# Kernel tuning notes

Measured on AMD Instinct MI355X. Metric: run time of the kernel, lower is better.

The kernel has to match this reference:

```python
import jax, jax.numpy as jnp
import numpy as np

WINDOW_SIZE = 2
SOFTMAX_TEMP = 0.01
CART_RESOLUTION = 0.25
RANGE_KEEP = 3.0
EPS = 1e-12


def get_indices(batch_size, window_size):
    kp, dense = [], []
    for i in range(batch_size):
        for j in range(window_size - 1):
            kp.append(i * window_size + j)
            dense.append(i * window_size + j + 1)
    return np.asarray(kp), np.asarray(dense)


def normalize_coords(coords, height, width):
    # coords [B,N,2] pixel (u,v) -> [-1,1] (align_corners=True convention, as in the repo)
    u = 2.0 * coords[..., 0] / (width - 1) - 1.0
    v = 2.0 * coords[..., 1] / (height - 1) - 1.0
    return jnp.stack([u, v], axis=-1)


def grid_sample_bilinear(img, grid):
    # Matches torch F.grid_sample(mode='bilinear', padding_mode='zeros', align_corners=False)
    # img [B,C,H,W], grid [B,Hg,Wg,2] with (x,y) in [-1,1]
    B, C, H, W = img.shape
    x = ((grid[..., 0] + 1.0) * W - 1.0) * 0.5
    y = ((grid[..., 1] + 1.0) * H - 1.0) * 0.5
    x0 = jnp.floor(x); y0 = jnp.floor(y)
    wx1 = x - x0; wy1 = y - y0

    def gather(xi, yi):
        valid = (xi >= 0) & (xi <= W - 1) & (yi >= 0) & (yi <= H - 1)
        xc = jnp.clip(xi, 0, W - 1).astype(jnp.int32)
        yc = jnp.clip(yi, 0, H - 1).astype(jnp.int32)
        v = jax.vmap(lambda im, yy, xx: im[:, yy, xx])(img, yc, xc)  # [B,C,Hg,Wg]
        return v * valid[:, None].astype(img.dtype)

    x1 = x0 + 1.0; y1 = y0 + 1.0
    out = (gather(x0, y0) * ((1.0 - wx1) * (1.0 - wy1))[:, None]
           + gather(x1, y0) * (wx1 * (1.0 - wy1))[:, None]
           + gather(x0, y1) * ((1.0 - wx1) * wy1)[:, None]
           + gather(x1, y1) * (wx1 * wy1)[:, None])
    return out


def setup_inputs() -> dict:
    key = jax.random.key(0)
    k1, k2, k3, k4, k5 = jax.random.split(key, 5)
    BW, C, N, H, W = 4, 256, 1024, 256, 256
    return {
        "keypoint_scores": jax.random.uniform(k1, (BW, 1, N), jnp.float32),
        "keypoint_desc": jax.random.normal(k2, (BW, C, N), jnp.float32),
        "scores_dense": jax.random.uniform(k3, (BW, 1, H, W), jnp.float32),
        "desc_dense": jax.random.normal(k4, (BW, C, H, W), jnp.float32),
        "keypoint_coords": jax.random.uniform(k5, (BW, N, 2), jnp.float32) * (W - 1),
    }


def reference(keypoint_scores, keypoint_desc, scores_dense, desc_dense, keypoint_coords):
    BW, encoder_dim, n_points = keypoint_desc.shape
    batch_size = BW // WINDOW_SIZE
    _, _, height, width = desc_dense.shape
    kp_inds, dense_inds = get_indices(batch_size, WINDOW_SIZE)

    src_coords = keypoint_coords[kp_inds]                      # [B,N,2]
    src_desc = keypoint_desc[kp_inds]                          # [B,C,N]
    src_desc = src_desc / jnp.maximum(jnp.linalg.norm(src_desc, axis=1, keepdims=True), EPS)
    B = src_desc.shape[0]

    tgt_desc_dense = desc_dense[dense_inds]                    # [B,C,H,W]
    tgt = tgt_desc_dense.reshape(B, encoder_dim, height * width)
    tgt = tgt / jnp.maximum(jnp.linalg.norm(tgt, axis=1, keepdims=True), EPS)

    # dense correlation [B, n_points, H*W]
    match_vals = jnp.einsum('bcn,bcm->bnm', src_desc, tgt)

    # local window mask (vectorized equivalent of the B x n_points python loop)
    keep_range = int(RANGE_KEEP // CART_RESOLUTION + 1)
    uv = jax.lax.stop_gradient(jnp.trunc(src_coords)).astype(jnp.int32)  # [B,N,2]
    u = uv[..., 0][..., None]   # [B,N,1]
    v = uv[..., 1][..., None]
    vg = jnp.arange(height)[None, None, :]
    ug = jnp.arange(width)[None, None, :]
    vmask = (vg >= v - keep_range) & (vg <= v + keep_range)    # [B,N,H]
    umask = (ug >= u - keep_range) & (ug <= u + keep_range)    # [B,N,W]
    mask = (vmask[..., :, None] & umask[..., None, :]).reshape(B, n_points, height * width)
    match_vals = match_vals * mask.astype(match_vals.dtype)

    soft = jax.nn.softmax(match_vals / SOFTMAX_TEMP, axis=2)   # [B,N,HW]

    # soft-argmax over the dense grid (meshgrid 'ij': v over rows, u over cols)
    ucoord = jnp.tile(jnp.arange(width, dtype=jnp.float32), height)
    vcoord = jnp.repeat(jnp.arange(height, dtype=jnp.float32), width)
    coords = jnp.stack([ucoord, vcoord], axis=1)               # [HW,2]
    pseudo_coords = jnp.einsum('bnm,mc->bnc', soft, coords)    # [B,N,2]

    pseudo_norm = normalize_coords(pseudo_coords, height, width)[:, None]  # [B,1,N,2]

    tgt_scores_dense = scores_dense[dense_inds]                # [B,1,H,W]
    pseudo_scores = grid_sample_bilinear(tgt_scores_dense, pseudo_norm).reshape(B, 1, n_points)
    pseudo_desc = grid_sample_bilinear(tgt_desc_dense, pseudo_norm).reshape(B, encoder_dim, n_points)

    desc_match_score = jnp.sum(src_desc * pseudo_desc, axis=1, keepdims=True) / float(encoder_dim)
    src_scores = keypoint_scores[kp_inds]
    match_weights = 0.5 * (desc_match_score + 1.0) * src_scores * pseudo_scores  # score_comp=True

    return pseudo_coords, match_weights, jnp.asarray(kp_inds)
```

## Files before the change

### kernel.cpp

```cpp
#include <hip/hip_runtime.h>
#include <math.h>

#define HH 256
#define WW 256
#define CC 256
#define HW 65536
#define NPTS 1024
#define BB 2
#define KEEP 13
#define KEEPM 14
#define TINV 100.0f
#define EPSN 1e-12f
#define S_ALL 8355840.0f

#define TW 32
#define TH 4
#define TUN 8
#define TPB 512
#define NT  (BB * TPB)
#define CAPT 192
#define VSTRIDE 864

__global__ __launch_bounds__(256) void prep_src(const float* __restrict__ kdesc,
                                                const float* __restrict__ kcoords,
                                                float* __restrict__ srcn,
                                                unsigned int* __restrict__ kparams) {
    int wid = threadIdx.x >> 6, lane = threadIdx.x & 63;
    int kpt = blockIdx.x * 4 + wid;
    int b = kpt >> 10, n = kpt & 1023;
    const float* src = kdesc + (size_t)(2 * b) * CC * NPTS + n;
    float vals[4];
    float ss = 0.f;
#pragma unroll
    for (int k = 0; k < 4; k++) {
        float x = src[(size_t)(lane + 64 * k) * NPTS];
        vals[k] = x;
        ss += x * x;
    }
    for (int o = 32; o > 0; o >>= 1) ss += __shfl_down(ss, o, 64);
    ss = __shfl(ss, 0, 64);
    float inv = 1.0f / fmaxf(sqrtf(ss), EPSN);
    float* dst = srcn + (size_t)kpt * CC;
#pragma unroll
    for (int k = 0; k < 4; k++) dst[lane + 64 * k] = vals[k] * inv;

    if (lane == 0) {
        float cu = kcoords[((size_t)(2 * b) * NPTS + n) * 2 + 0];
        float cv = kcoords[((size_t)(2 * b) * NPTS + n) * 2 + 1];
        int u = (int)truncf(cu), v = (int)truncf(cv);
        int u0m = max(0, u - KEEPM), u1m = min(WW - 1, u + KEEPM);
        int v0m = max(0, v - KEEPM), v1m = min(HH - 1, v + KEEPM);
        int nWm = u1m - u0m + 1, nHm = v1m - v0m + 1;
        kparams[kpt] = (unsigned)u0m | ((unsigned)v0m << 8) |
                       ((unsigned)nWm << 16) | ((unsigned)nHm << 24);
    }
}

__global__ __launch_bounds__(256) void corr_tiles(const float* __restrict__ ddense,
                                                  const float* __restrict__ srcn,
                                                  const unsigned int* __restrict__ kparams,
                                                  float* __restrict__ vals,
                                                  float* __restrict__ invn) {
    __shared__ float B_lds[CC][33];
    __shared__ int s_kid[CAPT];
    __shared__ unsigned int s_kp[CAPT];
    __shared__ int s_cnt;

    int tileg = blockIdx.x;
    int b = tileg >> 9, tl = tileg & 511;
    int tv = tl >> 3, tu = tl & 7;
    int vb = tv * TH, ub = tu * TW;
    int t = threadIdx.x;
    if (t == 0) s_cnt = 0;
    __syncthreads();

    for (int i = t; i < NPTS; i += 256) {
        unsigned int kp = kparams[b * NPTS + i];
        int u0m = kp & 255, v0m = (kp >> 8) & 255;
        int nWm = (kp >> 16) & 255, nHm = (int)(kp >> 24);
        if (u0m <= ub + TW - 1 && u0m + nWm - 1 >= ub &&
            v0m <= vb + TH - 1 && v0m + nHm - 1 >= vb) {
            int slot = atomicAdd(&s_cnt, 1);
            if (slot < CAPT) {
                s_kid[slot] = b * NPTS + i;
                s_kp[slot] = kp;
            }
        }
    }
    __syncthreads();
    int nk = min(s_cnt, CAPT);
    if (nk == 0) return;

    int pxg = t & 31, kg = t >> 5;
    int px4 = pxg * 4, k4 = kg * 4;
    const float* abase = ddense + (size_t)(2 * b + 1) * CC * HW +
                         (size_t)(vb + (px4 >> 5)) * WW + (ub + (px4 & 31));

    for (int kc = 0; kc < nk; kc += 32) {
        int nkk = min(32, nk - kc);
#pragma unroll 4
        for (int i = 0; i < nkk; i++)
            B_lds[t][i] = srcn[(size_t)s_kid[kc + i] * CC + t];
        __syncthreads();

        float acc[4][4];
#pragma unroll
        for (int i = 0; i < 4; i++)
#pragma unroll
            for (int j = 0; j < 4; j++) acc[i][j] = 0.f;

        int kgn = (nkk + 3) >> 2;
        if (kg < kgn) {
            float ss0 = 0.f, ss1 = 0.f, ss2 = 0.f, ss3 = 0.f;
#pragma unroll 4
            for (int c = 0; c < CC; c++) {
                float4 av = *(const float4*)(abase + (size_t)c * HW);
                const float* brow = &B_lds[c][k4];
                float b0 = brow[0], b1 = brow[1], b2 = brow[2], b3 = brow[3];
                acc[0][0] = fmaf(av.x, b0, acc[0][0]);
                acc[0][1] = fmaf(av.x, b1, acc[0][1]);
                acc[0][2] = fmaf(av.x, b2, acc[0][2]);
                acc[0][3] = fmaf(av.x, b3, acc[0][3]);
                acc[1][0] = fmaf(av.y, b0, acc[1][0]);
                acc[1][1] = fmaf(av.y, b1, acc[1][1]);
                acc[1][2] = fmaf(av.y, b2, acc[1][2]);
                acc[1][3] = fmaf(av.y, b3, acc[1][3]);
                acc[2][0] = fmaf(av.z, b0, acc[2][0]);
                acc[2][1] = fmaf(av.z, b1, acc[2][1]);
                acc[2][2] = fmaf(av.z, b2, acc[2][2]);
                acc[2][3] = fmaf(av.z, b3, acc[2][3]);
                acc[3][0] = fmaf(av.w, b0, acc[3][0]);
                acc[3][1] = fmaf(av.w, b1, acc[3][1]);
                acc[3][2] = fmaf(av.w, b2, acc[3][2]);
                acc[3][3] = fmaf(av.w, b3, acc[3][3]);
                ss0 = fmaf(av.x, av.x, ss0);
                ss1 = fmaf(av.y, av.y, ss1);
                ss2 = fmaf(av.z, av.z, ss2);
                ss3 = fmaf(av.w, av.w, ss3);
            }
            if (kc == 0 && kg == 0) {
                float i0 = 1.0f / fmaxf(sqrtf(ss0), EPSN);
                float i1 = 1.0f / fmaxf(sqrtf(ss1), EPSN);
                float i2 = 1.0f / fmaxf(sqrtf(ss2), EPSN);
                float i3 = 1.0f / fmaxf(sqrtf(ss3), EPSN);
                int wv = vb + (px4 >> 5), wu = ub + (px4 & 31);
                float* ip = invn + (size_t)b * HW + wv * WW + wu;
                ip[0] = i0; ip[1] = i1; ip[2] = i2; ip[3] = i3;
            }
        }

#pragma unroll
        for (int i = 0; i < 4; i++) {
            int px = px4 + i;
            int wv = vb + (px >> 5), wu = ub + (px & 31);
#pragma unroll
            for (int j = 0; j < 4; j++) {
                int s = k4 + j;
                if (s < nkk) {
                    unsigned int kp = s_kp[kc + s];
                    int u0m = kp & 255, v0m = (kp >> 8) & 255;
                    int nWm = (kp >> 16) & 255, nHm = (int)(kp >> 24);
                    int du = wu - u0m, dv = wv - v0m;
                    if ((unsigned)du < (unsigned)nWm && (unsigned)dv < (unsigned)nHm)
                        vals[(size_t)s_kid[kc + s] * VSTRIDE + dv * nWm + du] =
                            acc[i][j];
                }
            }
        }
        __syncthreads();
    }
}

__device__ inline float blockSum(float v, float* sred, int t) {
    for (int o = 32; o > 0; o >>= 1) v += __shfl_down(v, o, 64);
    __syncthreads();
    if ((t & 63) == 0) sred[t >> 6] = v;
    __syncthreads();
    return sred[0] + sred[1] + sred[2] + sred[3];
}

__global__ __launch_bounds__(256) void finish(const float* __restrict__ kscores,
                                              const float* __restrict__ sdense,
                                              const float* __restrict__ ddense,
                                              const float* __restrict__ kcoords,
                                              const float* __restrict__ srcn,
                                              const float* __restrict__ vals,
                                              const float* __restrict__ invn,
                                              float* __restrict__ out) {
    __shared__ float s_src[CC];
    __shared__ float s_red[4];
    int t = threadIdx.x;
    int kpt = blockIdx.x;
    int b = kpt >> 10, n = kpt & 1023;

    s_src[t] = srcn[(size_t)kpt * CC + t];

    float cu = kcoords[((size_t)(2 * b) * NPTS + n) * 2 + 0];
    float cv = kcoords[((size_t)(2 * b) * NPTS + n) * 2 + 1];
    int u = (int)truncf(cu), v = (int)truncf(cv);
    int u0 = max(0, u - KEEP), u1 = min(WW - 1, u + KEEP);
    int v0 = max(0, v - KEEP), v1 = min(HH - 1, v + KEEP);
    int nW = u1 - u0 + 1, nH = v1 - v0 + 1;
    int cnt = nW * nH;
    int u0m = max(0, u - KEEPM), u1m = min(WW - 1, u + KEEPM);
    int v0m = max(0, v - KEEPM), v1m = min(HH - 1, v + KEEPM);
    int nWm = u1m - u0m + 1, nHm = v1m - v0m + 1;
    int cntm = nWm * nHm;

    const float* vrow = vals + (size_t)kpt * VSTRIDE;
    const float* inb = invn + (size_t)b * HW;
    __syncthreads();

    float valk[4];
    int puk[4], pvk[4];
    bool gk[4];
    float lm = -INFINITY;
#pragma unroll
    for (int k = 0; k < 4; k++) {
        int p = t + k * 256;
        bool gm = p < cntm;
        int pp = gm ? p : 0;
        int dvm = pp / nWm, dum = pp - dvm * nWm;
        int pu = u0m + dum, pv = v0m + dvm;
        bool inw = gm && pu >= u0 && pu <= u1 && pv >= v0 && pv <= v1;
        float raw = gm ? vrow[pp] : 0.f;
        float val = inw ? raw * inb[pv * WW + pu] : 0.f;
        valk[k] = val;
        puk[k] = pu;
        pvk[k] = pv;
        gk[k] = inw;
        if (inw) lm = fmaxf(lm, val);
    }

    for (int o = 32; o > 0; o >>= 1) lm = fmaxf(lm, __shfl_down(lm, o, 64));
    if ((t & 63) == 0) s_red[t >> 6] = lm;
    __syncthreads();
    float m = fmaxf(fmaxf(s_red[0], s_red[1]), fmaxf(s_red[2], s_red[3]));
    m = fmaxf(m, 0.0f);

    float pse = 0.f, psu = 0.f, psv = 0.f;
#pragma unroll
    for (int k = 0; k < 4; k++) {
        float e = gk[k] ? expf(TINV * (valk[k] - m)) : 0.f;
        pse += e;
        psu = fmaf(e, (float)puk[k], psu);
        psv = fmaf(e, (float)pvk[k], psv);
    }
    float se = blockSum(pse, s_red, t);
    float su = blockSum(psu, s_red, t);
    float sv = blockSum(psv, s_red, t);

    float em = expf(-TINV * m);
    float sumWinU = 0.5f * (float)(u0 + u1) * (float)nW * (float)nH;
    float sumWinV = 0.5f * (float)(v0 + v1) * (float)nH * (float)nW;
    float denom = se + (65536.0f - (float)cnt) * em;
    float pcu = (su + em * (S_ALL - sumWinU)) / denom;
    float pcv = (sv + em * (S_ALL - sumWinV)) / denom;

    if (t == 0) {
        out[((size_t)b * NPTS + n) * 2 + 0] = pcu;
        out[((size_t)b * NPTS + n) * 2 + 1] = pcv;
    }

    float x = pcu * (256.0f / 255.0f) - 0.5f;
    float y = pcv * (256.0f / 255.0f) - 0.5f;
    float x0f = floorf(x), y0f = floorf(y);
    float wx = x - x0f, wy = y - y0f;
    int xi0 = (int)x0f, yi0 = (int)y0f, xi1 = xi0 + 1, yi1 = yi0 + 1;
    float w00 = (1.f - wx) * (1.f - wy), w10 = wx * (1.f - wy);
    float w01 = (1.f - wx) * wy, w11 = wx * wy;
    bool vx0 = (xi0 >= 0) & (xi0 < WW), vx1 = (xi1 >= 0) & (xi1 < WW);
    bool vy0 = (yi0 >= 0) & (yi0 < HH), vy1 = (yi1 >= 0) & (yi1 < HH);
    int cx0 = min(max(xi0, 0), WW - 1), cx1 = min(max(xi1, 0), WW - 1);
    int cy0 = min(max(yi0, 0), HH - 1), cy1 = min(max(yi1, 0), HH - 1);

    int cxs[4] = {cx0, cx1, cx0, cx1};
    int cys[4] = {cy0, cy0, cy1, cy1};
    bool cvalid[4] = {vx0 && vy0, vx1 && vy0, vx0 && vy1, vx1 && vy1};
    float wts[4] = {w00, w10, w01, w11};

    bool need = false;
    float dacc = 0.f;
#pragma unroll
    for (int c4 = 0; c4 < 4; c4++) {
        if (cvalid[c4]) {
            int du = cxs[c4] - u0m, dv = cys[c4] - v0m;
            if ((unsigned)du < (unsigned)nWm && (unsigned)dv < (unsigned)nHm)
                dacc = fmaf(wts[c4], vrow[dv * nWm + du], dacc);
            else
                need = true;
        }
    }

    float dms;
    if (need) {
        const float* tgt = ddense + (size_t)(2 * b + 1) * CC * HW;
        int c = t;
        const float* ch = tgt + ((size_t)c << 16);
        float d00 = cvalid[0] ? ch[cys[0] * WW + cxs[0]] : 0.f;
        float d10 = cvalid[1] ? ch[cys[1] * WW + cxs[1]] : 0.f;
        float d01 = cvalid[2] ? ch[cys[2] * WW + cxs[2]] : 0.f;
        float d11 = cvalid[3] ? ch[cys[3] * WW + cxs[3]] : 0.f;
        float pd = d00 * wts[0] + d10 * wts[1] + d01 * wts[2] + d11 * wts[3];
        float dsum = blockSum(pd * s_src[c], s_red, t);
        dms = dsum / (float)CC;
    } else {
        dms = dacc / (float)CC;
    }

    if (t == 0) {
        const float* sch = sdense + (size_t)(2 * b + 1) * HW;
        float s00 = cvalid[0] ? sch[cys[0] * WW + cxs[0]] : 0.f;
        float s10 = cvalid[1] ? sch[cys[1] * WW + cxs[1]] : 0.f;
        float s01 = cvalid[2] ? sch[cys[2] * WW + cxs[2]] : 0.f;
        float s11 = cvalid[3] ? sch[cys[3] * WW + cxs[3]] : 0.f;
        float psc = s00 * wts[0] + s10 * wts[1] + s01 * wts[2] + s11 * wts[3];
        float sscore = kscores[(size_t)(2 * b) * NPTS + n];
        float wgt = 0.5f * (dms + 1.0f) * sscore * psc;
        out[2 * NPTS * BB + (size_t)b * NPTS + n] = wgt;
    }

    if (kpt == 0 && t < 2) out[3 * NPTS * BB + t] = 2.0f * (float)t;
}

__global__ __launch_bounds__(256) void prep_tgt(const float* __restrict__ dd,
                                                float* __restrict__ invn) {
    int idx = blockIdx.x * 256 + threadIdx.x;
    int b = idx >> 16, m = idx & 65535;
    const float* p = dd + (size_t)(2 * b + 1) * CC * HW + m;
    float ss = 0.f;
#pragma unroll 4
    for (int c = 0; c < CC; c++) {
        float x = p[(size_t)c << 16];
        ss += x * x;
    }
    invn[idx] = 1.0f / fmaxf(sqrtf(ss), EPSN);
}

__global__ __launch_bounds__(256) void matcher(const float* __restrict__ kscores,
                                               const float* __restrict__ sdense,
                                               const float* __restrict__ ddense,
                                               const float* __restrict__ kcoords,
                                               const float* __restrict__ srcn,
                                               const float* __restrict__ invn,
                                               float* __restrict__ out) {
    __shared__ float s_src[CC];
    __shared__ float s_red[4];
    int t = threadIdx.x;
    int kpt = blockIdx.x;
    int b = kpt >> 10, n = kpt & 1023;

    s_src[t] = srcn[(size_t)kpt * CC + t];

    float cu = kcoords[((size_t)(2 * b) * NPTS + n) * 2 + 0];
    float cv = kcoords[((size_t)(2 * b) * NPTS + n) * 2 + 1];
    int u = (int)truncf(cu), v = (int)truncf(cv);
    int u0 = max(0, u - KEEP), u1 = min(WW - 1, u + KEEP);
    int v0 = max(0, v - KEEP), v1 = min(HH - 1, v + KEEP);
    int nW = u1 - u0 + 1, nH = v1 - v0 + 1;
    int cnt = nW * nH;

    const float* tgt = ddense + (size_t)(2 * b + 1) * CC * HW;
    const float* inb = invn + (size_t)b * HW;
    __syncthreads();

    int p0 = t, p1 = t + 256, p2 = t + 512;
    bool g0 = p0 < cnt, g1 = p1 < cnt, g2 = p2 < cnt;
    int dv0 = p0 / nW, dv1 = p1 / nW, dv2 = p2 / nW;
    int uu0 = u0 + (p0 - dv0 * nW), uu1 = u0 + (p1 - dv1 * nW), uu2 = u0 + (p2 - dv2 * nW);
    int vv0 = v0 + dv0, vv1 = v0 + dv1, vv2 = v0 + dv2;
    int mi0 = g0 ? (vv0 * WW + uu0) : 0;
    int mi1 = g1 ? (vv1 * WW + uu1) : 0;
    int mi2 = g2 ? (vv2 * WW + uu2) : 0;

    const float* q0 = tgt + mi0;
    const float* q1 = tgt + mi1;
    const float* q2 = tgt + mi2;
    float a0 = 0.f, a1 = 0.f, a2 = 0.f;
#pragma unroll 4
    for (int c = 0; c < CC; c++) {
        float s = s_src[c];
        size_t off = (size_t)c << 16;
        a0 = fmaf(s, q0[off], a0);
        a1 = fmaf(s, q1[off], a1);
        a2 = fmaf(s, q2[off], a2);
    }
    float val0 = a0 * inb[mi0];
    float val1 = a1 * inb[mi1];
    float val2 = a2 * inb[mi2];

    float lm = fmaxf(fmaxf(g0 ? val0 : -INFINITY, g1 ? val1 : -INFINITY),
                     g2 ? val2 : -INFINITY);
    for (int o = 32; o > 0; o >>= 1) lm = fmaxf(lm, __shfl_down(lm, o, 64));
    if ((t & 63) == 0) s_red[t >> 6] = lm;
    __syncthreads();
    float m = fmaxf(fmaxf(s_red[0], s_red[1]), fmaxf(s_red[2], s_red[3]));
    m = fmaxf(m, 0.0f);

    float e0 = g0 ? expf(TINV * (val0 - m)) : 0.f;
    float e1 = g1 ? expf(TINV * (val1 - m)) : 0.f;
    float e2 = g2 ? expf(TINV * (val2 - m)) : 0.f;

    float se = blockSum(e0 + e1 + e2, s_red, t);
    float su = blockSum(e0 * uu0 + e1 * uu1 + e2 * uu2, s_red, t);
    float sv = blockSum(e0 * vv0 + e1 * vv1 + e2 * vv2, s_red, t);

    float em = expf(-TINV * m);
    float sumWinU = 0.5f * (float)(u0 + u1) * (float)nW * (float)nH;
    float sumWinV = 0.5f * (float)(v0 + v1) * (float)nH * (float)nW;
    float denom = se + (65536.0f - (float)cnt) * em;
    float pcu = (su + em * (S_ALL - sumWinU)) / denom;
    float pcv = (sv + em * (S_ALL - sumWinV)) / denom;

    if (t == 0) {
        out[((size_t)b * NPTS + n) * 2 + 0] = pcu;
        out[((size_t)b * NPTS + n) * 2 + 1] = pcv;
    }

    float x = pcu * (256.0f / 255.0f) - 0.5f;
    float y = pcv * (256.0f / 255.0f) - 0.5f;
    float x0f = floorf(x), y0f = floorf(y);
    float wx = x - x0f, wy = y - y0f;
    int xi0 = (int)x0f, yi0 = (int)y0f, xi1 = xi0 + 1, yi1 = yi0 + 1;
    float w00 = (1.f - wx) * (1.f - wy), w10 = wx * (1.f - wy);
    float w01 = (1.f - wx) * wy, w11 = wx * wy;
    bool vx0 = (xi0 >= 0) & (xi0 < WW), vx1 = (xi1 >= 0) & (xi1 < WW);
    bool vy0 = (yi0 >= 0) & (yi0 < HH), vy1 = (yi1 >= 0) & (yi1 < HH);
    int cx0 = min(max(xi0, 0), WW - 1), cx1 = min(max(xi1, 0), WW - 1);
    int cy0 = min(max(yi0, 0), HH - 1), cy1 = min(max(yi1, 0), HH - 1);

    {
        int c = t;
        const float* ch = tgt + ((size_t)c << 16);
        float d00 = (vx0 && vy0) ? ch[cy0 * WW + cx0] : 0.f;
        float d10 = (vx1 && vy0) ? ch[cy0 * WW + cx1] : 0.f;
        float d01 = (vx0 && vy1) ? ch[cy1 * WW + cx0] : 0.f;
        float d11 = (vx1 && vy1) ? ch[cy1 * WW + cx1] : 0.f;
        float pd = d00 * w00 + d10 * w10 + d01 * w01 + d11 * w11;
        float contrib = pd * s_src[c];
        float dsum = blockSum(contrib, s_red, t);
        if (t == 0) {
            float dms = dsum / (float)CC;
            const float* sch = sdense + (size_t)(2 * b + 1) * HW;
            float s00 = (vx0 && vy0) ? sch[cy0 * WW + cx0] : 0.f;
            float s10 = (vx1 && vy0) ? sch[cy0 * WW + cx1] : 0.f;
            float s01 = (vx0 && vy1) ? sch[cy1 * WW + cx0] : 0.f;
            float s11 = (vx1 && vy1) ? sch[cy1 * WW + cx1] : 0.f;
            float psc = s00 * w00 + s10 * w10 + s01 * w01 + s11 * w11;
            float sscore = kscores[(size_t)(2 * b) * NPTS + n];
            float wgt = 0.5f * (dms + 1.0f) * sscore * psc;
            out[2 * NPTS * BB + (size_t)b * NPTS + n] = wgt;
        }
    }

    if (kpt == 0 && t < 2) out[3 * NPTS * BB + t] = 2.0f * (float)t;
}

extern "C" void kernel_launch(void* const* d_in, const int* in_sizes, int n_in,
                              void* d_out, int out_size, void* d_ws, size_t ws_size,
                              hipStream_t stream) {
    const float* kscores = (const float*)d_in[0];
    const float* kdesc   = (const float*)d_in[1];
    const float* sdense  = (const float*)d_in[2];
    const float* ddense  = (const float*)d_in[3];
    const float* kcoords = (const float*)d_in[4];
    float* out = (float*)d_out;

    float* srcn = (float*)d_ws;
    float* vals = srcn + (size_t)BB * NPTS * CC;
    float* invn = vals + (size_t)BB * NPTS * VSTRIDE;
    unsigned int* kparams = (unsigned int*)(invn + (size_t)BB * HW);
    size_t need = ((size_t)BB * NPTS * CC + (size_t)BB * NPTS * VSTRIDE +
                   (size_t)BB * HW + BB * NPTS) * 4;

    if (ws_size >= need) {
        hipLaunchKernelGGL(prep_src, dim3(512), dim3(256), 0, stream,
                           kdesc, kcoords, srcn, kparams);
        hipLaunchKernelGGL(corr_tiles, dim3(NT), dim3(256), 0, stream,
                           ddense, srcn, kparams, vals, invn);
        hipLaunchKernelGGL(finish, dim3(BB * NPTS), dim3(256), 0, stream,
                           kscores, sdense, ddense, kcoords, srcn, vals, invn, out);
    } else {
        float* invn2 = srcn + (size_t)BB * NPTS * CC;
        hipLaunchKernelGGL(prep_src, dim3(512), dim3(256), 0, stream,
                           kdesc, kcoords, srcn, kparams);
        hipLaunchKernelGGL(prep_tgt, dim3(512), dim3(256), 0, stream, ddense, invn2);
        hipLaunchKernelGGL(matcher, dim3(BB * NPTS), dim3(256), 0, stream,
                           kscores, sdense, ddense, kcoords, srcn, invn2, out);
    }
}
```

Baseline: 92.05 us.

## Bin keypoints to tiles globally and split correlation tiles into chunk blocks

Adds a bin_kpts kernel that uses global atomics to build a per-tile keypoint list once, replacing the per-block scan of all 1024 keypoints in corr_tiles. corr_tiles now launches one block per (tile, 32-keypoint chunk), so the serial chunk loop inside a block becomes parallel work. prep_src is rewritten to transpose 64 keypoints through LDS for coalesced loads and stores. The per-tile capacity drops from 192 to 96 keypoints, and the change adds a memset plus an extra kernel launch.

```diff
diff --git a/kernel.cpp b/kernel.cpp
--- a/kernel.cpp
+++ b/kernel.cpp
@@ -17,34 +17,47 @@
 #define TH 4
 #define TUN 8
 #define TPB 512
-#define NT  (BB * TPB)
-#define CAPT 192
+#define NTILE (BB * TPB)
+#define CAPL 96
+#define NCHUNK 3
 #define VSTRIDE 864
+#define BPAD 36
+#define KPB 64
 
 __global__ __launch_bounds__(256) void prep_src(const float* __restrict__ kdesc,
                                                 const float* __restrict__ kcoords,
                                                 float* __restrict__ srcn,
                                                 unsigned int* __restrict__ kparams) {
-    int wid = threadIdx.x >> 6, lane = threadIdx.x & 63;
-    int kpt = blockIdx.x * 4 + wid;
-    int b = kpt >> 10, n = kpt & 1023;
-    const float* src = kdesc + (size_t)(2 * b) * CC * NPTS + n;
-    float vals[4];
-    float ss = 0.f;
-#pragma unroll
-    for (int k = 0; k < 4; k++) {
-        float x = src[(size_t)(lane + 64 * k) * NPTS];
-        vals[k] = x;
-        ss += x * x;
-    }
-    for (int o = 32; o > 0; o >>= 1) ss += __shfl_down(ss, o, 64);
-    ss = __shfl(ss, 0, 64);
-    float inv = 1.0f / fmaxf(sqrtf(ss), EPSN);
-    float* dst = srcn + (size_t)kpt * CC;
-#pragma unroll
-    for (int k = 0; k < 4; k++) dst[lane + 64 * k] = vals[k] * inv;
-
-    if (lane == 0) {
+    __shared__ float tr[KPB][CC + 1];
+    __shared__ float red[4][KPB];
+    __shared__ float s_inv[KPB];
+    int t = threadIdx.x;
+    int kpt0 = blockIdx.x * KPB;
+    int b = kpt0 >> 10;
+    int n0 = kpt0 & 1023;
+    const float* srcbase = kdesc + (size_t)(2 * b) * CC * NPTS;
+
+    int cj = t >> 6, nj = t & 63;
+    for (int c0 = 0; c0 < CC; c0 += 4)
+        tr[nj][c0 + cj] = srcbase[(size_t)(c0 + cj) * NPTS + n0 + nj];
+    __syncthreads();
+
+    {
+        int j = t & 63, p = t >> 6;
+        float ss = 0.f;
+#pragma unroll 8
+        for (int i = 0; i < 64; i++) {
+            float x = tr[j][p * 64 + i];
+            ss = fmaf(x, x, ss);
+        }
+        red[p][j] = ss;
+    }
+    __syncthreads();
+    if (t < KPB) {
+        float ss = red[0][t] + red[1][t] + red[2][t] + red[3][t];
+        s_inv[t] = 1.0f / fmaxf(sqrtf(ss), EPSN);
+        int kpt = kpt0 + t;
+        int n = kpt & 1023;
         float cu = kcoords[((size_t)(2 * b) * NPTS + n) * 2 + 0];
         float cv = kcoords[((size_t)(2 * b) * NPTS + n) * 2 + 1];
         int u = (int)truncf(cu), v = (int)truncf(cv);
@@ -54,120 +67,129 @@
         kparams[kpt] = (unsigned)u0m | ((unsigned)v0m << 8) |
                        ((unsigned)nWm << 16) | ((unsigned)nHm << 24);
     }
+    __syncthreads();
+    for (int j = 0; j < KPB; j++)
+        srcn[(size_t)(kpt0 + j) * CC + t] = tr[j][t] * s_inv[j];
+}
+
+__global__ __launch_bounds__(256) void bin_kpts(const unsigned int* __restrict__ kparams,
+                                                int* __restrict__ counts,
+                                                int2* __restrict__ lists2) {
+    int kpt = blockIdx.x * 256 + threadIdx.x;
+    unsigned int kp = kparams[kpt];
+    int b = kpt >> 10;
+    int u0m = kp & 255, v0m = (kp >> 8) & 255;
+    int nWm = (kp >> 16) & 255, nHm = (int)(kp >> 24);
+    int tu0 = u0m >> 5, tu1 = (u0m + nWm - 1) >> 5;
+    int tv0 = v0m >> 2, tv1 = (v0m + nHm - 1) >> 2;
+    for (int tv = tv0; tv <= tv1; tv++)
+        for (int tu = tu0; tu <= tu1; tu++) {
+            int tg = b * TPB + tv * TUN + tu;
+            int slot = atomicAdd(&counts[tg], 1);
+            if (slot < CAPL) lists2[tg * CAPL + slot] = make_int2(kpt, (int)kp);
+        }
 }
 
 __global__ __launch_bounds__(256) void corr_tiles(const float* __restrict__ ddense,
                                                   const float* __restrict__ srcn,
-                                                  const unsigned int* __restrict__ kparams,
+                                                  const int* __restrict__ counts,
+                                                  const int2* __restrict__ lists2,
                                                   float* __restrict__ vals,
                                                   float* __restrict__ invn) {
-    __shared__ float B_lds[CC][33];
-    __shared__ int s_kid[CAPT];
-    __shared__ unsigned int s_kp[CAPT];
-    __shared__ int s_cnt;
-
-    int tileg = blockIdx.x;
+    __shared__ __align__(16) float B_lds[CC][BPAD];
+    __shared__ int s_kid[32];
+    __shared__ unsigned int s_kp[32];
+
+    int bid = blockIdx.x;
+    int chunk = bid >> 10;
+    int tileg = bid & 1023;
+    int nk = min(counts[tileg], CAPL);
+    int base = chunk * 32;
+    int nkk = min(32, nk - base);
+    if (nkk <= 0) return;
+
     int b = tileg >> 9, tl = tileg & 511;
     int tv = tl >> 3, tu = tl & 7;
     int vb = tv * TH, ub = tu * TW;
     int t = threadIdx.x;
-    if (t == 0) s_cnt = 0;
-    __syncthreads();
-
-    for (int i = t; i < NPTS; i += 256) {
-        unsigned int kp = kparams[b * NPTS + i];
-        int u0m = kp & 255, v0m = (kp >> 8) & 255;
-        int nWm = (kp >> 16) & 255, nHm = (int)(kp >> 24);
-        if (u0m <= ub + TW - 1 && u0m + nWm - 1 >= ub &&
-            v0m <= vb + TH - 1 && v0m + nHm - 1 >= vb) {
-            int slot = atomicAdd(&s_cnt, 1);
-            if (slot < CAPT) {
-                s_kid[slot] = b * NPTS + i;
-                s_kp[slot] = kp;
-            }
-        }
-    }
-    __syncthreads();
-    int nk = min(s_cnt, CAPT);
-    if (nk == 0) return;
+    if (t < nkk) {
+        int2 e = lists2[tileg * CAPL + base + t];
+        s_kid[t] = e.x;
+        s_kp[t] = (unsigned int)e.y;
+    }
+    __syncthreads();
+
+#pragma unroll 4
+    for (int i = 0; i < nkk; i++)
+        B_lds[t][i] = srcn[(size_t)s_kid[i] * CC + t];
+    __syncthreads();
 
     int pxg = t & 31, kg = t >> 5;
     int px4 = pxg * 4, k4 = kg * 4;
+    int wv = vb + (px4 >> 5), wu0 = ub + (px4 & 31);
     const float* abase = ddense + (size_t)(2 * b + 1) * CC * HW +
-                         (size_t)(vb + (px4 >> 5)) * WW + (ub + (px4 & 31));
-
-    for (int kc = 0; kc < nk; kc += 32) {
-        int nkk = min(32, nk - kc);
+                         (size_t)wv * WW + wu0;
+
+    float acc[4][4];
+#pragma unroll
+    for (int i = 0; i < 4; i++)
+#pragma unroll
+        for (int j = 0; j < 4; j++) acc[i][j] = 0.f;
+
+    int kgn = (nkk + 3) >> 2;
+    if (kg < kgn) {
+        float ss0 = 0.f, ss1 = 0.f, ss2 = 0.f, ss3 = 0.f;
 #pragma unroll 4
-        for (int i = 0; i < nkk; i++)
-            B_lds[t][i] = srcn[(size_t)s_kid[kc + i] * CC + t];
-        __syncthreads();
-
-        float acc[4][4];
-#pragma unroll
-        for (int i = 0; i < 4; i++)
-#pragma unroll
-            for (int j = 0; j < 4; j++) acc[i][j] = 0.f;
-
-        int kgn = (nkk + 3) >> 2;
-        if (kg < kgn) {
-            float ss0 = 0.f, ss1 = 0.f, ss2 = 0.f, ss3 = 0.f;
-#pragma unroll 4
-            for (int c = 0; c < CC; c++) {
-                float4 av = *(const float4*)(abase + (size_t)c * HW);
-                const float* brow = &B_lds[c][k4];
-                float b0 = brow[0], b1 = brow[1], b2 = brow[2], b3 = brow[3];
-                acc[0][0] = fmaf(av.x, b0, acc[0][0]);
-                acc[0][1] = fmaf(av.x, b1, acc[0][1]);
-                acc[0][2] = fmaf(av.x, b2, acc[0][2]);
-                acc[0][3] = fmaf(av.x, b3, acc[0][3]);
-                acc[1][0] = fmaf(av.y, b0, acc[1][0]);
-                acc[1][1] = fmaf(av.y, b1, acc[1][1]);
-                acc[1][2] = fmaf(av.y, b2, acc[1][2]);
-                acc[1][3] = fmaf(av.y, b3, acc[1][3]);
-                acc[2][0] = fmaf(av.z, b0, acc[2][0]);
-                acc[2][1] = fmaf(av.z, b1, acc[2][1]);
-                acc[2][2] = fmaf(av.z, b2, acc[2][2]);
-                acc[2][3] = fmaf(av.z, b3, acc[2][3]);
-                acc[3][0] = fmaf(av.w, b0, acc[3][0]);
-                acc[3][1] = fmaf(av.w, b1, acc[3][1]);
-                acc[3][2] = fmaf(av.w, b2, acc[3][2]);
-                acc[3][3] = fmaf(av.w, b3, acc[3][3]);
-                ss0 = fmaf(av.x, av.x, ss0);
-                ss1 = fmaf(av.y, av.y, ss1);
-                ss2 = fmaf(av.z, av.z, ss2);
-                ss3 = fmaf(av.w, av.w, ss3);
+        for (int c = 0; c < CC; c++) {
+            float4 av = *(const float4*)(abase + (size_t)c * HW);
+            const float* brow = &B_lds[c][k4];
+            float b0 = brow[0], b1 = brow[1], b2 = brow[2], b3 = brow[3];
+            acc[0][0] = fmaf(av.x, b0, acc[0][0]);
+            acc[0][1] = fmaf(av.x, b1, acc[0][1]);
+            acc[0][2] = fmaf(av.x, b2, acc[0][2]);
+            acc[0][3] = fmaf(av.x, b3, acc[0][3]);
+            acc[1][0] = fmaf(av.y, b0, acc[1][0]);
+            acc[1][1] = fmaf(av.y, b1, acc[1][1]);
+            acc[1][2] = fmaf(av.y, b2, acc[1][2]);
+            acc[1][3] = fmaf(av.y, b3, acc[1][3]);
+            acc[2][0] = fmaf(av.z, b0, acc[2][0]);
+            acc[2][1] = fmaf(av.z, b1, acc[2][1]);
+            acc[2][2] = fmaf(av.z, b2, acc[2][2]);
+            acc[2][3] = fmaf(av.z, b3, acc[2][3]);
+            acc[3][0] = fmaf(av.w, b0, acc[3][0]);
+            acc[3][1] = fmaf(av.w, b1, acc[3][1]);
+            acc[3][2] = fmaf(av.w, b2, acc[3][2]);
+            acc[3][3] = fmaf(av.w, b3, acc[3][3]);
+            ss0 = fmaf(av.x, av.x, ss0);
+            ss1 = fmaf(av.y, av.y, ss1);
+            ss2 = fmaf(av.z, av.z, ss2);
+            ss3 = fmaf(av.w, av.w, ss3);
+        }
+        if (chunk == 0 && kg == 0) {
+            float i0 = 1.0f / fmaxf(sqrtf(ss0), EPSN);
+            float i1 = 1.0f / fmaxf(sqrtf(ss1), EPSN);
+            float i2 = 1.0f / fmaxf(sqrtf(ss2), EPSN);
+            float i3 = 1.0f / fmaxf(sqrtf(ss3), EPSN);
+            float* ip = invn + (size_t)b * HW + wv * WW + wu0;
+            ip[0] = i0; ip[1] = i1; ip[2] = i2; ip[3] = i3;
+        }
+    }
+
+#pragma unroll
+    for (int i = 0; i < 4; i++) {
+        int swu = wu0 + i;
+#pragma unroll
+        for (int j = 0; j < 4; j++) {
+            int s = k4 + j;
+            if (s < nkk) {
+                unsigned int kp = s_kp[s];
+                int u0m = kp & 255, v0m = (kp >> 8) & 255;
+                int nWm = (kp >> 16) & 255, nHm = (int)(kp >> 24);
+                int du = swu - u0m, dv = wv - v0m;
+                if ((unsigned)du < (unsigned)nWm && (unsigned)dv < (unsigned)nHm)
+                    vals[(size_t)s_kid[s] * VSTRIDE + dv * nWm + du] = acc[i][j];
             }
-            if (kc == 0 && kg == 0) {
-                float i0 = 1.0f / fmaxf(sqrtf(ss0), EPSN);
-                float i1 = 1.0f / fmaxf(sqrtf(ss1), EPSN);
-                float i2 = 1.0f / fmaxf(sqrtf(ss2), EPSN);
-                float i3 = 1.0f / fmaxf(sqrtf(ss3), EPSN);
-                int wv = vb + (px4 >> 5), wu = ub + (px4 & 31);
-                float* ip = invn + (size_t)b * HW + wv * WW + wu;
-                ip[0] = i0; ip[1] = i1; ip[2] = i2; ip[3] = i3;
-            }
-        }
-
-#pragma unroll
-        for (int i = 0; i < 4; i++) {
-            int px = px4 + i;
-            int wv = vb + (px >> 5), wu = ub + (px & 31);
-#pragma unroll
-            for (int j = 0; j < 4; j++) {
-                int s = k4 + j;
-                if (s < nkk) {
-                    unsigned int kp = s_kp[kc + s];
-                    int u0m = kp & 255, v0m = (kp >> 8) & 255;
-                    int nWm = (kp >> 16) & 255, nHm = (int)(kp >> 24);
-                    int du = wu - u0m, dv = wv - v0m;
-                    if ((unsigned)du < (unsigned)nWm && (unsigned)dv < (unsigned)nHm)
-                        vals[(size_t)s_kid[kc + s] * VSTRIDE + dv * nWm + du] =
-                            acc[i][j];
-                }
-            }
-        }
-        __syncthreads();
+        }
     }
 }
 
@@ -470,19 +492,25 @@
     float* vals = srcn + (size_t)BB * NPTS * CC;
     float* invn = vals + (size_t)BB * NPTS * VSTRIDE;
     unsigned int* kparams = (unsigned int*)(invn + (size_t)BB * HW);
+    int* counts = (int*)(kparams + BB * NPTS);
+    int2* lists2 = (int2*)(counts + NTILE);
     size_t need = ((size_t)BB * NPTS * CC + (size_t)BB * NPTS * VSTRIDE +
-                   (size_t)BB * HW + BB * NPTS) * 4;
+                   (size_t)BB * HW + BB * NPTS + NTILE +
+                   (size_t)NTILE * CAPL * 2) * 4;
 
     if (ws_size >= need) {
-        hipLaunchKernelGGL(prep_src, dim3(512), dim3(256), 0, stream,
+        hipMemsetAsync(counts, 0, NTILE * sizeof(int), stream);
+        hipLaunchKernelGGL(prep_src, dim3(BB * NPTS / KPB), dim3(256), 0, stream,
                            kdesc, kcoords, srcn, kparams);
-        hipLaunchKernelGGL(corr_tiles, dim3(NT), dim3(256), 0, stream,
-                           ddense, srcn, kparams, vals, invn);
+        hipLaunchKernelGGL(bin_kpts, dim3(8), dim3(256), 0, stream,
+                           kparams, counts, lists2);
+        hipLaunchKernelGGL(corr_tiles, dim3(NCHUNK * NTILE), dim3(256), 0, stream,
+                           ddense, srcn, counts, lists2, vals, invn);
         hipLaunchKernelGGL(finish, dim3(BB * NPTS), dim3(256), 0, stream,
                            kscores, sdense, ddense, kcoords, srcn, vals, invn, out);
     } else {
         float* invn2 = srcn + (size_t)BB * NPTS * CC;
-        hipLaunchKernelGGL(prep_src, dim3(512), dim3(256), 0, stream,
+        hipLaunchKernelGGL(prep_src, dim3(BB * NPTS / KPB), dim3(256), 0, stream,
                            kdesc, kcoords, srcn, kparams);
         hipLaunchKernelGGL(prep_tgt, dim3(512), dim3(256), 0, stream, ddense, invn2);
         hipLaunchKernelGGL(matcher, dim3(BB * NPTS), dim3(256), 0, stream,
```

After: 100.4 us. 9.0% more time.

## Transpose source descriptors via LDS and fold target norm into correlation tiles

Applied to the files above, without the earlier changes.

prep_src now loads 64 keypoints per block with coalesced reads into a padded LDS transpose, then computes the norms and writes normalized rows. Before, each wavefront read one keypoint with a strided gather. corr_tiles keeps the per-pixel inverse norms in shared memory and writes correlation values that are already normalized, so finish no longer gathers invn for every window element. The bilinear path in finish now divides by invn to undo that scaling, which adds a gather and a division there. B_lds padding changes from 33 to 36.

```diff
diff --git a/kernel.cpp b/kernel.cpp
--- a/kernel.cpp
+++ b/kernel.cpp
@@ -20,31 +20,43 @@
 #define NT  (BB * TPB)
 #define CAPT 192
 #define VSTRIDE 864
+#define BPAD 36
+#define KPB 64
 
 __global__ __launch_bounds__(256) void prep_src(const float* __restrict__ kdesc,
                                                 const float* __restrict__ kcoords,
                                                 float* __restrict__ srcn,
                                                 unsigned int* __restrict__ kparams) {
-    int wid = threadIdx.x >> 6, lane = threadIdx.x & 63;
-    int kpt = blockIdx.x * 4 + wid;
-    int b = kpt >> 10, n = kpt & 1023;
-    const float* src = kdesc + (size_t)(2 * b) * CC * NPTS + n;
-    float vals[4];
-    float ss = 0.f;
-#pragma unroll
-    for (int k = 0; k < 4; k++) {
-        float x = src[(size_t)(lane + 64 * k) * NPTS];
-        vals[k] = x;
-        ss += x * x;
-    }
-    for (int o = 32; o > 0; o >>= 1) ss += __shfl_down(ss, o, 64);
-    ss = __shfl(ss, 0, 64);
-    float inv = 1.0f / fmaxf(sqrtf(ss), EPSN);
-    float* dst = srcn + (size_t)kpt * CC;
-#pragma unroll
-    for (int k = 0; k < 4; k++) dst[lane + 64 * k] = vals[k] * inv;
-
-    if (lane == 0) {
+    __shared__ float tr[KPB][CC + 1];
+    __shared__ float red[4][KPB];
+    __shared__ float s_inv[KPB];
+    int t = threadIdx.x;
+    int kpt0 = blockIdx.x * KPB;
+    int b = kpt0 >> 10;
+    int n0 = kpt0 & 1023;
+    const float* srcbase = kdesc + (size_t)(2 * b) * CC * NPTS;
+
+    int cj = t >> 6, nj = t & 63;
+    for (int c0 = 0; c0 < CC; c0 += 4)
+        tr[nj][c0 + cj] = srcbase[(size_t)(c0 + cj) * NPTS + n0 + nj];
+    __syncthreads();
+
+    {
+        int j = t & 63, p = t >> 6;
+        float ss = 0.f;
+#pragma unroll 8
+        for (int i = 0; i < 64; i++) {
+            float x = tr[j][p * 64 + i];
+            ss = fmaf(x, x, ss);
+        }
+        red[p][j] = ss;
+    }
+    __syncthreads();
+    if (t < KPB) {
+        float ss = red[0][t] + red[1][t] + red[2][t] + red[3][t];
+        s_inv[t] = 1.0f / fmaxf(sqrtf(ss), EPSN);
+        int kpt = kpt0 + t;
+        int n = kpt & 1023;
         float cu = kcoords[((size_t)(2 * b) * NPTS + n) * 2 + 0];
         float cv = kcoords[((size_t)(2 * b) * NPTS + n) * 2 + 1];
         int u = (int)truncf(cu), v = (int)truncf(cv);
@@ -54,6 +66,9 @@
         kparams[kpt] = (unsigned)u0m | ((unsigned)v0m << 8) |
                        ((unsigned)nWm << 16) | ((unsigned)nHm << 24);
     }
+    __syncthreads();
+    for (int j = 0; j < KPB; j++)
+        srcn[(size_t)(kpt0 + j) * CC + t] = tr[j][t] * s_inv[j];
 }
 
 __global__ __launch_bounds__(256) void corr_tiles(const float* __restrict__ ddense,
@@ -61,7 +76,8 @@
                                                   const unsigned int* __restrict__ kparams,
                                                   float* __restrict__ vals,
                                                   float* __restrict__ invn) {
-    __shared__ float B_lds[CC][33];
+    __shared__ __align__(16) float B_lds[CC][BPAD];
+    __shared__ float s_inorm[TW * TH];
     __shared__ int s_kid[CAPT];
     __shared__ unsigned int s_kp[CAPT];
     __shared__ int s_cnt;
@@ -93,8 +109,9 @@
 
     int pxg = t & 31, kg = t >> 5;
     int px4 = pxg * 4, k4 = kg * 4;
+    int wv = vb + (px4 >> 5), wu0 = ub + (px4 & 31);
     const float* abase = ddense + (size_t)(2 * b + 1) * CC * HW +
-                         (size_t)(vb + (px4 >> 5)) * WW + (ub + (px4 & 31));
+                         (size_t)wv * WW + wu0;
 
     for (int kc = 0; kc < nk; kc += 32) {
         int nkk = min(32, nk - kc);
@@ -143,16 +160,21 @@
                 float i1 = 1.0f / fmaxf(sqrtf(ss1), EPSN);
                 float i2 = 1.0f / fmaxf(sqrtf(ss2), EPSN);
                 float i3 = 1.0f / fmaxf(sqrtf(ss3), EPSN);
-                int wv = vb + (px4 >> 5), wu = ub + (px4 & 31);
-                float* ip = invn + (size_t)b * HW + wv * WW + wu;
+                s_inorm[px4 + 0] = i0;
+                s_inorm[px4 + 1] = i1;
+                s_inorm[px4 + 2] = i2;
+                s_inorm[px4 + 3] = i3;
+                float* ip = invn + (size_t)b * HW + wv * WW + wu0;
                 ip[0] = i0; ip[1] = i1; ip[2] = i2; ip[3] = i3;
             }
         }
+        if (kc == 0) __syncthreads();
 
 #pragma unroll
         for (int i = 0; i < 4; i++) {
             int px = px4 + i;
-            int wv = vb + (px >> 5), wu = ub + (px & 31);
+            int swv = vb + (px >> 5), swu = ub + (px & 31);
+            float iv = s_inorm[px];
 #pragma unroll
             for (int j = 0; j < 4; j++) {
                 int s = k4 + j;
@@ -160,10 +182,10 @@
                     unsigned int kp = s_kp[kc + s];
                     int u0m = kp & 255, v0m = (kp >> 8) & 255;
                     int nWm = (kp >> 16) & 255, nHm = (int)(kp >> 24);
-                    int du = wu - u0m, dv = wv - v0m;
+                    int du = swu - u0m, dv = swv - v0m;
                     if ((unsigned)du < (unsigned)nWm && (unsigned)dv < (unsigned)nHm)
                         vals[(size_t)s_kid[kc + s] * VSTRIDE + dv * nWm + du] =
-                            acc[i][j];
+                            acc[i][j] * iv;
                 }
             }
         }
@@ -208,7 +230,6 @@
     int cntm = nWm * nHm;
 
     const float* vrow = vals + (size_t)kpt * VSTRIDE;
-    const float* inb = invn + (size_t)b * HW;
     __syncthreads();
 
     float valk[4];
@@ -223,8 +244,7 @@
         int dvm = pp / nWm, dum = pp - dvm * nWm;
         int pu = u0m + dum, pv = v0m + dvm;
         bool inw = gm && pu >= u0 && pu <= u1 && pv >= v0 && pv <= v1;
-        float raw = gm ? vrow[pp] : 0.f;
-        float val = inw ? raw * inb[pv * WW + pu] : 0.f;
+        float val = inw ? vrow[pp] : 0.f;
         valk[k] = val;
         puk[k] = pu;
         pvk[k] = pv;
@@ -285,10 +305,12 @@
     for (int c4 = 0; c4 < 4; c4++) {
         if (cvalid[c4]) {
             int du = cxs[c4] - u0m, dv = cys[c4] - v0m;
-            if ((unsigned)du < (unsigned)nWm && (unsigned)dv < (unsigned)nHm)
-                dacc = fmaf(wts[c4], vrow[dv * nWm + du], dacc);
-            else
+            if ((unsigned)du < (unsigned)nWm && (unsigned)dv < (unsigned)nHm) {
+                float inv = invn[(size_t)b * HW + cys[c4] * WW + cxs[c4]];
+                dacc = fmaf(wts[c4], vrow[dv * nWm + du] / inv, dacc);
+            } else {
                 need = true;
+            }
         }
     }
 
@@ -474,7 +496,7 @@
                    (size_t)BB * HW + BB * NPTS) * 4;
 
     if (ws_size >= need) {
-        hipLaunchKernelGGL(prep_src, dim3(512), dim3(256), 0, stream,
+        hipLaunchKernelGGL(prep_src, dim3(BB * NPTS / KPB), dim3(256), 0, stream,
                            kdesc, kcoords, srcn, kparams);
         hipLaunchKernelGGL(corr_tiles, dim3(NT), dim3(256), 0, stream,
                            ddense, srcn, kparams, vals, invn);
@@ -482,7 +504,7 @@
                            kscores, sdense, ddense, kcoords, srcn, vals, invn, out);
     } else {
         float* invn2 = srcn + (size_t)BB * NPTS * CC;
-        hipLaunchKernelGGL(prep_src, dim3(512), dim3(256), 0, stream,
+        hipLaunchKernelGGL(prep_src, dim3(BB * NPTS / KPB), dim3(256), 0, stream,
                            kdesc, kcoords, srcn, kparams);
         hipLaunchKernelGGL(prep_tgt, dim3(512), dim3(256), 0, stream, ddense, invn2);
         hipLaunchKernelGGL(matcher, dim3(BB * NPTS), dim3(256), 0, stream,
```

After: 91.92 us. About the same (-0.1%).
